# Optimization experiments

Hardware: AMD Instinct MI355X
Metric: run time of the kernel (lower is better)

Reference implementation:

```python
import jax, jax.numpy as jnp
import numpy as np

B, S, FEAT, HID, H = 8, 1024, 1024, 1024, 8
DH = HID // H  # head dim = 128
MASK_VAL = -128.0  # mask_val = -2**7 (soft additive mask, per original code)


def setup_inputs() -> dict:
    key = jax.random.key(0)
    ks = jax.random.split(key, 4)
    scale = 0.02
    return {
        "queries": jax.random.normal(ks[0], (B, S, FEAT), dtype=jnp.float32),
        "Wq": jax.random.normal(ks[1], (FEAT, HID), dtype=jnp.float32) * scale,
        "bq": jnp.zeros((HID,), dtype=jnp.float32),
        "Wk": jax.random.normal(ks[2], (FEAT, HID), dtype=jnp.float32) * scale,
        "bk": jnp.zeros((HID,), dtype=jnp.float32),
        "Wv": jax.random.normal(ks[3], (FEAT, HID), dtype=jnp.float32) * scale,
        "bv": jnp.zeros((HID,), dtype=jnp.float32),
    }


def reference(queries, Wq, bq, Wk, bk, Wv, bv):
    # Self-attention: keys = values = queries (torch forward defaults)
    q = queries @ Wq + bq  # [B,S,HID]
    k = queries @ Wk + bk
    v = queries @ Wv + bv
    # split heads: chunk along last dim == reshape (B,S,H,DH)
    qh = q.reshape(B, S, H, DH)
    kh = k.reshape(B, S, H, DH)
    vh = v.reshape(B, S, H, DH)
    # exp-scaled-dot score (non-standard: exp BEFORE mask/softmax)
    logits = jnp.einsum("bqhd,bkhd->bhqk", qh, kh) / np.float32(np.sqrt(DH))
    score = jnp.exp(logits)
    # soft additive causal mask: upper triangle (diag=1) gets -128
    mask = jnp.triu(jnp.full((S, S), MASK_VAL, dtype=score.dtype), k=1)
    att = jax.nn.softmax(score + mask, axis=-1)  # [B,H,S,S]
    ctx = jnp.einsum("bhqk,bkhd->bqhd", att, vh)  # [B,S,H,DH]
    # reverse heads: concat along last dim
    return ctx.reshape(B, S, HID)
```

## Files before the change

kernel.cpp:

```cpp
#include <hip/hip_runtime.h>


typedef __bf16 bf16x8 __attribute__((ext_vector_type(8)));
typedef float floatx4 __attribute__((ext_vector_type(4)));
typedef unsigned short u16;

#define RSCALE 0.08838834764831845f

__device__ __forceinline__ u16 f2b(float f) {
  union { float f; unsigned u; } v; v.f = f;
  return (u16)((v.u + 0x7FFFu + ((v.u >> 16) & 1u)) >> 16);
}

__device__ __forceinline__ void gld_lds16(const void* g, void* l) {
  __builtin_amdgcn_global_load_lds(
      (const __attribute__((address_space(1))) unsigned*)g,
      (__attribute__((address_space(3))) unsigned*)l, 16, 0, 0);
}

#define MFMA16(a, b, c) __builtin_amdgcn_mfma_f32_16x16x32_bf16(a, b, c, 0, 0, 0)

__global__ __launch_bounds__(256) void cast_x_kernel(const float4* __restrict__ X,
                                                     u16* __restrict__ Xb) {
  unsigned i = blockIdx.x * 256u + threadIdx.x;
  float4 v = X[i];
  ushort4 o;
  o.x = f2b(v.x); o.y = f2b(v.y); o.z = f2b(v.z); o.w = f2b(v.w);
  *reinterpret_cast<ushort4*>(Xb + 4u * i) = o;
}

__global__ __launch_bounds__(256) void transpose_w_kernel(
    const float* __restrict__ Wq, const float* __restrict__ Wk,
    const float* __restrict__ Wv, u16* __restrict__ Wtb) {
  const float* W = (blockIdx.z == 0) ? Wq : (blockIdx.z == 1) ? Wk : Wv;
  u16* Wt = Wtb + (size_t)blockIdx.z * (1024u * 1024u);
  __shared__ u16 tile[32][33];
  const int x = threadIdx.x, y = threadIdx.y;
  const int kt = blockIdx.x * 32, nt = blockIdx.y * 32;
#pragma unroll
  for (int i = 0; i < 4; ++i)
    tile[y + 8 * i][x] = f2b(W[(size_t)(kt + y + 8 * i) * 1024 + nt + x]);
  __syncthreads();
#pragma unroll
  for (int i = 0; i < 4; ++i)
    Wt[(size_t)(nt + y + 8 * i) * 1024 + kt + x] = tile[x][y + 8 * i];
}

__global__ __launch_bounds__(256) void gemm_qkv_kernel(
    const u16* __restrict__ Xb, const u16* __restrict__ Wtb,
    const float* __restrict__ bq, const float* __restrict__ bk,
    const float* __restrict__ bv, u16* __restrict__ Qh, u16* __restrict__ Kh,
    u16* __restrict__ Vt) {
  const int mat = blockIdx.z;
  const u16* __restrict__ Wt = Wtb + (size_t)mat * (1024u * 1024u);
  const float* __restrict__ bias = (mat == 0) ? bq : (mat == 1) ? bk : bv;

  const int m0 = blockIdx.x * 128;
  const int n0 = blockIdx.y * 128;

  __shared__ u16 As[128 * 32];
  __shared__ u16 Bs[128 * 32];

  const int tid = threadIdx.x;
  const int wid = tid >> 6;
  const int lane = tid & 63;
  const int quad = lane >> 4;
  const int l16 = lane & 15;
  const int wm = (wid & 1) * 64;
  const int wn = (wid >> 1) * 64;

  const floatx4 z4 = {0.f, 0.f, 0.f, 0.f};
  floatx4 acc[4][4];
#pragma unroll
  for (int i = 0; i < 4; ++i)
#pragma unroll
    for (int j = 0; j < 4; ++j) acc[i][j] = z4;

  const int rbase = wid * 32;
  for (int k0 = 0; k0 < 1024; k0 += 32) {
    __syncthreads();
#pragma unroll
    for (int c = 0; c < 2; ++c) {
      const int row = rbase + c * 16 + (lane >> 2);
      const int kk = k0 + (lane & 3) * 8;
      gld_lds16(Xb + (size_t)(m0 + row) * 1024 + kk, As + (rbase + c * 16) * 32);
      gld_lds16(Wt + (size_t)(n0 + row) * 1024 + kk, Bs + (rbase + c * 16) * 32);
    }
    __syncthreads();

    bf16x8 af[4], bfr[4];
#pragma unroll
    for (int i = 0; i < 4; ++i)
      af[i] = *(const bf16x8*)(As + (wm + i * 16 + l16) * 32 + quad * 8);
#pragma unroll
    for (int j = 0; j < 4; ++j)
      bfr[j] = *(const bf16x8*)(Bs + (wn + j * 16 + l16) * 32 + quad * 8);
#pragma unroll
    for (int i = 0; i < 4; ++i)
#pragma unroll
      for (int j = 0; j < 4; ++j) acc[i][j] = MFMA16(af[i], bfr[j], acc[i][j]);
  }

  const int b = m0 >> 10;
  const int h = n0 >> 7;
  const int sbase = (m0 & 1023) + wm;
  float bv4[4];
#pragma unroll
  for (int j = 0; j < 4; ++j) bv4[j] = bias[n0 + wn + j * 16 + l16];

  if (mat < 2) {
    u16* outp = (mat == 0 ? Qh : Kh) + (size_t)(b * 8 + h) * 1024 * 128;
#pragma unroll
    for (int i = 0; i < 4; ++i)
#pragma unroll
      for (int j = 0; j < 4; ++j) {
        const int d = wn + j * 16 + l16;
#pragma unroll
        for (int r = 0; r < 4; ++r) {
          const int s = sbase + i * 16 + quad * 4 + r;
          outp[(size_t)s * 128 + d] = f2b(acc[i][j][r] + bv4[j]);
        }
      }
  } else {
    u16* outp = Vt + (size_t)(b * 8 + h) * 128 * 1024;
#pragma unroll
    for (int i = 0; i < 4; ++i)
#pragma unroll
      for (int j = 0; j < 4; ++j) {
        const int d = wn + j * 16 + l16;
        const int s = sbase + i * 16 + quad * 4;
        ushort4 pk;
        pk.x = f2b(acc[i][j][0] + bv4[j]);
        pk.y = f2b(acc[i][j][1] + bv4[j]);
        pk.z = f2b(acc[i][j][2] + bv4[j]);
        pk.w = f2b(acc[i][j][3] + bv4[j]);
        *(ushort4*)(outp + (size_t)d * 1024 + s) = pk;
      }
  }
}

__global__ __launch_bounds__(256) void attn_kernel(const u16* __restrict__ Qh,
                                                   const u16* __restrict__ Kh,
                                                   const u16* __restrict__ Vt,
                                                   float* __restrict__ out) {
  const int bh = blockIdx.x;
  const int q0 = blockIdx.y * 128;
  const int tid = threadIdx.x;
  const int wid = tid >> 6;
  const int lane = tid & 63;
  const int quad = lane >> 4;
  const int l16 = lane & 15;

  __shared__ u16 Ks[32 * 128];
  __shared__ u16 Vs[128 * 32];
  __shared__ u16 Ps[4 * 32 * 32];

  const u16* __restrict__ Qbase = Qh + (size_t)bh * 1024 * 128;
  const u16* __restrict__ Kbase = Kh + (size_t)bh * 1024 * 128;
  const u16* __restrict__ Vbase = Vt + (size_t)bh * 128 * 1024;

  const int qw = q0 + wid * 32;

  bf16x8 qf[2][4];
#pragma unroll
  for (int mt = 0; mt < 2; ++mt)
#pragma unroll
    for (int c = 0; c < 4; ++c)
      qf[mt][c] = *(const bf16x8*)(Qbase + (size_t)(qw + mt * 16 + l16) * 128 +
                                   c * 32 + quad * 8);

  const floatx4 z4 = {0.f, 0.f, 0.f, 0.f};
  floatx4 o[2][8];
#pragma unroll
  for (int mt = 0; mt < 2; ++mt)
#pragma unroll
    for (int dt = 0; dt < 8; ++dt) o[mt][dt] = z4;
  float lacc[2][4] = {};

  const int kend = q0 + 128;
  for (int k0 = 0; k0 < kend; k0 += 32) {
    __syncthreads();
#pragma unroll
    for (int c = 0; c < 2; ++c) {
      const int row = wid * 8 + c * 4 + (lane >> 4);
      const int gb = (lane & 15) ^ (row & 15);
      gld_lds16(Kbase + (size_t)(k0 + row) * 128 + gb * 8,
                Ks + (wid * 8 + c * 4) * 128);
    }
#pragma unroll
    for (int c = 0; c < 2; ++c) {
      const int row = wid * 32 + c * 16 + (lane >> 2);
      const int kk = k0 + (lane & 3) * 8;
      gld_lds16(Vbase + (size_t)row * 1024 + kk, Vs + (wid * 32 + c * 16) * 32);
    }
    __syncthreads();

    bf16x8 kf[2][4];
#pragma unroll
    for (int nt = 0; nt < 2; ++nt)
#pragma unroll
      for (int c = 0; c < 4; ++c)
        kf[nt][c] = *(const bf16x8*)(Ks + (nt * 16 + l16) * 128 +
                                     (((c * 4 + quad) ^ l16) * 8));

#pragma unroll
    for (int mt = 0; mt < 2; ++mt) {
      floatx4 s0 = z4, s1 = z4;
#pragma unroll
      for (int c = 0; c < 4; ++c) {
        s0 = MFMA16(qf[mt][c], kf[0][c], s0);
        s1 = MFMA16(qf[mt][c], kf[1][c], s1);
      }
#pragma unroll
      for (int r = 0; r < 4; ++r) {
        const int qrow = qw + mt * 16 + quad * 4 + r;
        const float e0 = fminf(__expf(s0[r] * RSCALE), 85.f);
        const float e1 = fminf(__expf(s1[r] * RSCALE), 85.f);
        const float p0 = (k0 + l16 > qrow) ? 0.f : __expf(e0);
        const float p1 = (k0 + 16 + l16 > qrow) ? 0.f : __expf(e1);
        lacc[mt][r] += p0 + p1;
        Ps[wid * 1024 + (mt * 16 + quad * 4 + r) * 32 + l16] = f2b(p0);
        Ps[wid * 1024 + (mt * 16 + quad * 4 + r) * 32 + 16 + l16] = f2b(p1);
      }
    }
    asm volatile("s_waitcnt lgkmcnt(0)" ::: "memory");

    bf16x8 pa[2];
#pragma unroll
    for (int mt = 0; mt < 2; ++mt)
      pa[mt] = *(const bf16x8*)(Ps + wid * 1024 + (mt * 16 + l16) * 32 + quad * 8);
#pragma unroll
    for (int dt = 0; dt < 8; ++dt) {
      const bf16x8 vf = *(const bf16x8*)(Vs + (dt * 16 + l16) * 32 + quad * 8);
      o[0][dt] = MFMA16(pa[0], vf, o[0][dt]);
      o[1][dt] = MFMA16(pa[1], vf, o[1][dt]);
    }
  }

  float linv[2][4];
#pragma unroll
  for (int mt = 0; mt < 2; ++mt)
#pragma unroll
    for (int r = 0; r < 4; ++r) {
      float s = lacc[mt][r];
      s += __shfl_xor(s, 1, 16);
      s += __shfl_xor(s, 2, 16);
      s += __shfl_xor(s, 4, 16);
      s += __shfl_xor(s, 8, 16);
      linv[mt][r] = 1.0f / s;
    }

  float* outp = out + ((size_t)(bh >> 3) * 1024) * 1024 + (bh & 7) * 128;
#pragma unroll
  for (int mt = 0; mt < 2; ++mt)
#pragma unroll
    for (int dt = 0; dt < 8; ++dt)
#pragma unroll
      for (int r = 0; r < 4; ++r) {
        const int qrow = qw + mt * 16 + quad * 4 + r;
        outp[(size_t)qrow * 1024 + dt * 16 + l16] = o[mt][dt][r] * linv[mt][r];
      }
}

extern "C" void kernel_launch(void* const* d_in, const int* in_sizes, int n_in,
                              void* d_out, int out_size, void* d_ws,
                              size_t ws_size, hipStream_t stream) {
  const float* X = (const float*)d_in[0];
  const float* Wq = (const float*)d_in[1];
  const float* bq = (const float*)d_in[2];
  const float* Wk = (const float*)d_in[3];
  const float* bk = (const float*)d_in[4];
  const float* Wv = (const float*)d_in[5];
  const float* bv = (const float*)d_in[6];
  float* out = (float*)d_out;

  char* ws = (char*)d_ws;
  u16* Xb  = (u16*)(ws);
  u16* Wtb = (u16*)(ws + (16u << 20));
  u16* Qh  = (u16*)(ws + (22u << 20));
  u16* Kh  = (u16*)(ws + (38u << 20));
  u16* Vt  = (u16*)(ws + (54u << 20));

  cast_x_kernel<<<8192, 256, 0, stream>>>((const float4*)X, Xb);
  dim3 gt(32, 32, 3), bt(32, 8);
  transpose_w_kernel<<<gt, bt, 0, stream>>>(Wq, Wk, Wv, Wtb);
  dim3 gg(64, 8, 3);
  gemm_qkv_kernel<<<gg, 256, 0, stream>>>(Xb, Wtb, bq, bk, bv, Qh, Kh, Vt);
  dim3 ga(64, 8);
  attn_kernel<<<ga, 256, 0, stream>>>(Qh, Kh, Vt, out);
}
```

Measured before the change: 225.7 us.

## Widen K tiles to 64, swizzle LDS, double-buffer K in attention

The QKV GEMM now stages K-chunks of 64 instead of 32, using an XOR-swizzled LDS layout. This halves the number of barriers per output tile and avoids bank conflicts. The attention kernel processes 64-key blocks and double-buffers K tiles, prefetching the next tile while the current one is being computed. It waits with a partial vmcnt so the loads overlap the exp/MFMA work. It also reverses the query-tile launch order so the longest causal blocks start first, and swizzles the P and V LDS buffers. LDS use roughly doubles, which may lower occupancy, and the hand-written waitcnt counts must match the number of outstanding loads exactly.

```diff
diff --git a/kernel.cpp b/kernel.cpp
--- a/kernel.cpp
+++ b/kernel.cpp
@@ -58,14 +58,15 @@
   const int m0 = blockIdx.x * 128;
   const int n0 = blockIdx.y * 128;
 
-  __shared__ u16 As[128 * 32];
-  __shared__ u16 Bs[128 * 32];
+  __shared__ u16 As[128 * 64];
+  __shared__ u16 Bs[128 * 64];
 
   const int tid = threadIdx.x;
   const int wid = tid >> 6;
   const int lane = tid & 63;
   const int quad = lane >> 4;
   const int l16 = lane & 15;
+  const int l8 = lane & 7;
   const int wm = (wid & 1) * 64;
   const int wn = (wid >> 1) * 64;
 
@@ -76,29 +77,37 @@
 #pragma unroll
     for (int j = 0; j < 4; ++j) acc[i][j] = z4;
 
-  const int rbase = wid * 32;
-  for (int k0 = 0; k0 < 1024; k0 += 32) {
+  const int srow = wid * 32;
+  const int lrow = lane >> 3;
+  const int gblk = l8 ^ lrow;
+
+  for (int k0 = 0; k0 < 1024; k0 += 64) {
     __syncthreads();
 #pragma unroll
+    for (int c = 0; c < 4; ++c) {
+      const int row = srow + c * 8 + lrow;
+      gld_lds16(Xb + (size_t)(m0 + row) * 1024 + k0 + gblk * 8,
+                As + (srow + c * 8) * 64);
+      gld_lds16(Wt + (size_t)(n0 + row) * 1024 + k0 + gblk * 8,
+                Bs + (srow + c * 8) * 64);
+    }
+    __syncthreads();
+
+#pragma unroll
     for (int c = 0; c < 2; ++c) {
-      const int row = rbase + c * 16 + (lane >> 2);
-      const int kk = k0 + (lane & 3) * 8;
-      gld_lds16(Xb + (size_t)(m0 + row) * 1024 + kk, As + (rbase + c * 16) * 32);
-      gld_lds16(Wt + (size_t)(n0 + row) * 1024 + kk, Bs + (rbase + c * 16) * 32);
-    }
-    __syncthreads();
-
-    bf16x8 af[4], bfr[4];
-#pragma unroll
-    for (int i = 0; i < 4; ++i)
-      af[i] = *(const bf16x8*)(As + (wm + i * 16 + l16) * 32 + quad * 8);
-#pragma unroll
-    for (int j = 0; j < 4; ++j)
-      bfr[j] = *(const bf16x8*)(Bs + (wn + j * 16 + l16) * 32 + quad * 8);
-#pragma unroll
-    for (int i = 0; i < 4; ++i)
-#pragma unroll
-      for (int j = 0; j < 4; ++j) acc[i][j] = MFMA16(af[i], bfr[j], acc[i][j]);
+      const int phys = ((c * 4 + quad) ^ (l16 & 7)) * 8;
+      bf16x8 af[4], bfr[4];
+#pragma unroll
+      for (int i = 0; i < 4; ++i)
+        af[i] = *(const bf16x8*)(As + (wm + i * 16 + l16) * 64 + phys);
+#pragma unroll
+      for (int j = 0; j < 4; ++j)
+        bfr[j] = *(const bf16x8*)(Bs + (wn + j * 16 + l16) * 64 + phys);
+#pragma unroll
+      for (int i = 0; i < 4; ++i)
+#pragma unroll
+        for (int j = 0; j < 4; ++j) acc[i][j] = MFMA16(af[i], bfr[j], acc[i][j]);
+    }
   }
 
   const int b = m0 >> 10;
@@ -144,16 +153,18 @@
                                                    const u16* __restrict__ Vt,
                                                    float* __restrict__ out) {
   const int bh = blockIdx.x;
-  const int q0 = blockIdx.y * 128;
+  const int qt = 7 - (int)blockIdx.y;
+  const int q0 = qt * 128;
   const int tid = threadIdx.x;
   const int wid = tid >> 6;
   const int lane = tid & 63;
   const int quad = lane >> 4;
   const int l16 = lane & 15;
-
-  __shared__ u16 Ks[32 * 128];
-  __shared__ u16 Vs[128 * 32];
-  __shared__ u16 Ps[4 * 32 * 32];
+  const int l8 = lane & 7;
+
+  __shared__ u16 Ks[2][64 * 128];
+  __shared__ u16 Vs[128 * 64];
+  __shared__ u16 Ps[4 * 32 * 64];
 
   const u16* __restrict__ Qbase = Qh + (size_t)bh * 1024 * 128;
   const u16* __restrict__ Kbase = Kh + (size_t)bh * 1024 * 128;
@@ -177,64 +188,88 @@
     for (int dt = 0; dt < 8; ++dt) o[mt][dt] = z4;
   float lacc[2][4] = {};
 
-  const int kend = q0 + 128;
-  for (int k0 = 0; k0 < kend; k0 += 32) {
+  const int n = (q0 + 128) >> 6;
+
+
+  {
+    const int kgb = l16 ^ quad;
+#pragma unroll
+    for (int c = 0; c < 4; ++c) {
+      const int row = wid * 16 + c * 4 + quad;
+      gld_lds16(Kbase + (size_t)row * 128 + (l16 ^ (c * 4 + quad)) * 8,
+                Ks[0] + (wid * 16 + c * 4) * 128);
+    }
+    (void)kgb;
+  }
+
+  for (int i = 0; i < n; ++i) {
+    const int k0 = i << 6;
     __syncthreads();
-#pragma unroll
-    for (int c = 0; c < 2; ++c) {
-      const int row = wid * 8 + c * 4 + (lane >> 4);
-      const int gb = (lane & 15) ^ (row & 15);
-      gld_lds16(Kbase + (size_t)(k0 + row) * 128 + gb * 8,
-                Ks + (wid * 8 + c * 4) * 128);
-    }
-#pragma unroll
-    for (int c = 0; c < 2; ++c) {
-      const int row = wid * 32 + c * 16 + (lane >> 2);
-      const int kk = k0 + (lane & 3) * 8;
-      gld_lds16(Vbase + (size_t)row * 1024 + kk, Vs + (wid * 32 + c * 16) * 32);
-    }
-    __syncthreads();
-
-    bf16x8 kf[2][4];
-#pragma unroll
-    for (int nt = 0; nt < 2; ++nt)
+
+#pragma unroll
+    for (int c = 0; c < 4; ++c) {
+      const int row = wid * 32 + c * 8 + (lane >> 3);
+      gld_lds16(Vbase + (size_t)row * 1024 + k0 + (l8 ^ (lane >> 3)) * 8,
+                Vs + (wid * 32 + c * 8) * 64);
+    }
+    if (i + 1 < n) {
+#pragma unroll
+      for (int c = 0; c < 4; ++c) {
+        const int row = wid * 16 + c * 4 + quad;
+        gld_lds16(Kbase + (size_t)(k0 + 64 + row) * 128 +
+                      (l16 ^ (c * 4 + quad)) * 8,
+                  Ks[(i + 1) & 1] + (wid * 16 + c * 4) * 128);
+      }
+    }
+
+    const u16* Kbuf = Ks[i & 1];
+#pragma unroll
+    for (int nt = 0; nt < 4; ++nt) {
+      bf16x8 kfc[4];
 #pragma unroll
       for (int c = 0; c < 4; ++c)
-        kf[nt][c] = *(const bf16x8*)(Ks + (nt * 16 + l16) * 128 +
-                                     (((c * 4 + quad) ^ l16) * 8));
-
-#pragma unroll
-    for (int mt = 0; mt < 2; ++mt) {
-      floatx4 s0 = z4, s1 = z4;
-#pragma unroll
-      for (int c = 0; c < 4; ++c) {
-        s0 = MFMA16(qf[mt][c], kf[0][c], s0);
-        s1 = MFMA16(qf[mt][c], kf[1][c], s1);
-      }
-#pragma unroll
-      for (int r = 0; r < 4; ++r) {
-        const int qrow = qw + mt * 16 + quad * 4 + r;
-        const float e0 = fminf(__expf(s0[r] * RSCALE), 85.f);
-        const float e1 = fminf(__expf(s1[r] * RSCALE), 85.f);
-        const float p0 = (k0 + l16 > qrow) ? 0.f : __expf(e0);
-        const float p1 = (k0 + 16 + l16 > qrow) ? 0.f : __expf(e1);
-        lacc[mt][r] += p0 + p1;
-        Ps[wid * 1024 + (mt * 16 + quad * 4 + r) * 32 + l16] = f2b(p0);
-        Ps[wid * 1024 + (mt * 16 + quad * 4 + r) * 32 + 16 + l16] = f2b(p1);
-      }
-    }
-    asm volatile("s_waitcnt lgkmcnt(0)" ::: "memory");
-
-    bf16x8 pa[2];
+        kfc[c] = *(const bf16x8*)(Kbuf + (nt * 16 + l16) * 128 +
+                                  (((c * 4 + quad) ^ l16) * 8));
+#pragma unroll
+      for (int mt = 0; mt < 2; ++mt) {
+        floatx4 s = z4;
+#pragma unroll
+        for (int c = 0; c < 4; ++c) s = MFMA16(qf[mt][c], kfc[c], s);
+#pragma unroll
+        for (int r = 0; r < 4; ++r) {
+          const int qrow = qw + mt * 16 + quad * 4 + r;
+          const int key = k0 + nt * 16 + l16;
+          const float e = fminf(__expf(s[r] * RSCALE), 85.f);
+          const float p = (key > qrow) ? 0.f : __expf(e);
+          lacc[mt][r] += p;
+          const int rowl = mt * 16 + quad * 4 + r;
+          const int phys = (nt * 2 + (l16 >> 3)) ^ (rowl & 7);
+          Ps[wid * 2048 + rowl * 64 + phys * 8 + (l16 & 7)] = f2b(p);
+        }
+      }
+    }
+
+    if (i + 1 < n)
+      asm volatile("s_waitcnt vmcnt(4) lgkmcnt(0)\n\ts_barrier" ::: "memory");
+    else
+      asm volatile("s_waitcnt vmcnt(0) lgkmcnt(0)\n\ts_barrier" ::: "memory");
+
+    bf16x8 pa[2][2];
 #pragma unroll
     for (int mt = 0; mt < 2; ++mt)
-      pa[mt] = *(const bf16x8*)(Ps + wid * 1024 + (mt * 16 + l16) * 32 + quad * 8);
-#pragma unroll
-    for (int dt = 0; dt < 8; ++dt) {
-      const bf16x8 vf = *(const bf16x8*)(Vs + (dt * 16 + l16) * 32 + quad * 8);
-      o[0][dt] = MFMA16(pa[0], vf, o[0][dt]);
-      o[1][dt] = MFMA16(pa[1], vf, o[1][dt]);
-    }
+#pragma unroll
+      for (int ck = 0; ck < 2; ++ck)
+        pa[mt][ck] = *(const bf16x8*)(Ps + wid * 2048 + (mt * 16 + l16) * 64 +
+                                      (((ck * 4 + quad) ^ (l16 & 7)) * 8));
+#pragma unroll
+    for (int dt = 0; dt < 8; ++dt)
+#pragma unroll
+      for (int ck = 0; ck < 2; ++ck) {
+        const bf16x8 vf = *(const bf16x8*)(Vs + (dt * 16 + l16) * 64 +
+                                           (((ck * 4 + quad) ^ (l16 & 7)) * 8));
+        o[0][dt] = MFMA16(pa[0][ck], vf, o[0][dt]);
+        o[1][dt] = MFMA16(pa[1][ck], vf, o[1][dt]);
+      }
   }
 
   float linv[2][4];
```

Measured after the change: 204.7 us. -9.3%, faster.
